# Kernel tuning notes

Measured on AMD Instinct MI355X. Metric: run time of the kernel, lower is better.

## Reference

```python
import jax, jax.numpy as jnp
import numpy as np

EMBED_DIM = 256
NUM_HEADS = 8
PROJ_DIM = EMBED_DIM // NUM_HEADS


def setup_inputs() -> dict:
    key = jax.random.key(0)
    ks = jax.random.split(key, 5)
    scale = 1.0 / np.sqrt(EMBED_DIM)
    inputs = jax.random.normal(ks[0], (2, 12, 12, 12, EMBED_DIM), dtype=jnp.float32)
    Wq = jax.random.normal(ks[1], (EMBED_DIM, EMBED_DIM), dtype=jnp.float32) * scale
    Wk = jax.random.normal(ks[2], (EMBED_DIM, EMBED_DIM), dtype=jnp.float32) * scale
    Wv = jax.random.normal(ks[3], (EMBED_DIM, EMBED_DIM), dtype=jnp.float32) * scale
    Wo = jax.random.normal(ks[4], (EMBED_DIM, EMBED_DIM), dtype=jnp.float32) * scale
    z = jnp.zeros((EMBED_DIM,), dtype=jnp.float32)
    return {"inputs": inputs, "Wq": Wq, "bq": z, "Wk": Wk, "bk": z,
            "Wv": Wv, "bv": z, "Wo": Wo, "bo": z}


def reference(inputs, Wq, bq, Wk, bk, Wv, bv, Wo, bo):
    B, h, w, d, E = inputs.shape
    S = h * w * d  # flattened spatial sequence
    x = inputs.reshape(B, S, E)
    # projections + head split: [B, S, E] -> [B, H, S, P]
    def split_heads(t):
        return t.reshape(B, S, NUM_HEADS, PROJ_DIM).transpose(0, 2, 1, 3)
    q = split_heads(x @ Wq + bq)
    k = split_heads(x @ Wk + bk)
    v = split_heads(x @ Wv + bv)
    # NOTE: original module does NOT scale by 1/sqrt(proj_dim)
    scores = jnp.einsum('bhsp,bhtp->bhst', q, k)  # [B, H, S, S]
    attn = jax.nn.softmax(scores, axis=-1)
    out = jnp.einsum('bhst,bhtp->bhsp', attn, v)  # [B, H, S, P]
    out = out.transpose(0, 2, 1, 3).reshape(B, h, w, d, E)
    return out @ Wo + bo
```

## Files before the change

kernel.cpp:

```cpp
#include <hip/hip_runtime.h>
#include <math.h>

#define EMBED 256
#define HEADS 8
#define PDIM  32
#define BATCH 2
#define SEQ   1728
#define NTOK  (BATCH*SEQ)
#define NE    (NTOK*EMBED)
#define KVB   128
#define NMAIN 13
#define TAIL0 1664
#define LOG2E 1.44269504088896f

typedef __attribute__((ext_vector_type(8))) __bf16 bf16x8;
typedef __attribute__((ext_vector_type(4))) float  f32x4;
typedef unsigned short ushort_t;
typedef unsigned int   uint_t;

static __device__ __forceinline__ unsigned short f2bf_rne(float f) {
    union { float f; unsigned u; } x; x.f = f;
    unsigned r = x.u + 0x7fffu + ((x.u >> 16) & 1u);
    return (unsigned short)(r >> 16);
}
union v8cast { uint4 u; bf16x8 v; };

static __device__ __forceinline__ void cvt8_hilo(const float f[8], bf16x8& hi, bf16x8& lo) {
    uint4 ph, pl;
    uint_t* phv = (uint_t*)&ph; uint_t* plv = (uint_t*)&pl;
    #pragma unroll
    for (int j = 0; j < 4; ++j) {
        const float f0 = f[2 * j], f1 = f[2 * j + 1];
        const uint_t u0 = __float_as_uint(f0) + 0x8000u;
        const uint_t u1 = __float_as_uint(f1) + 0x8000u;
        phv[j] = __builtin_amdgcn_perm(u1, u0, 0x07060302u);
        const float l0 = f0 - __uint_as_float(u0 & 0xFFFF0000u);
        const float l1 = f1 - __uint_as_float(u1 & 0xFFFF0000u);
        plv[j] = __builtin_amdgcn_perm(__float_as_uint(l1) + 0x8000u,
                                       __float_as_uint(l0) + 0x8000u, 0x07060302u);
    }
    v8cast ch; ch.u = ph; hi = ch.v;
    v8cast cl; cl.u = pl; lo = cl.v;
}

__global__ __launch_bounds__(256) void qkv_gemm_kernel(
    const float* __restrict__ x,
    const float* __restrict__ Wq, const float* __restrict__ bq,
    const float* __restrict__ Wk, const float* __restrict__ bk,
    const float* __restrict__ Wv, const float* __restrict__ bv,
    ushort_t* __restrict__ qo, ushort_t* __restrict__ ko, ushort_t* __restrict__ vt)
{
    const int t = threadIdx.x;
    const int lane = t & 63, li = lane & 15, quad = lane >> 4;
    const int w = t >> 6, wm = w >> 1, wn = w & 1;
    const int m0 = blockIdx.x * 64, n0 = blockIdx.y * 64, z = blockIdx.z;
    const float* __restrict__ W    = (z == 0) ? Wq : (z == 1) ? Wk : Wv;
    const float* __restrict__ bias = (z == 0) ? bq : (z == 1) ? bk : bv;

    __shared__ ushort_t Ah[2][64][40];
    __shared__ ushort_t Al[2][64][40];
    __shared__ ushort_t Bh[2][64][40];
    __shared__ ushort_t Bl[2][64][40];

    const int ar = t >> 2, ac = (t & 3) * 8;
    const int bn = t & 63, bk8 = (t >> 6) * 8;

    const float* agp = x + (size_t)(m0 + ar) * EMBED + ac;
    const float* bgp = W + (size_t)bk8 * EMBED + n0 + bn;

    float areg[8], breg[8];
    *(float4*)&areg[0] = *(const float4*)(agp);
    *(float4*)&areg[4] = *(const float4*)(agp + 4);
    #pragma unroll
    for (int j = 0; j < 8; ++j) breg[j] = bgp[(size_t)j * EMBED];

    f32x4 acc[2][2];
    #pragma unroll
    for (int mt = 0; mt < 2; ++mt)
        #pragma unroll
        for (int nt = 0; nt < 2; ++nt)
            acc[mt][nt] = (f32x4){0.f, 0.f, 0.f, 0.f};

    for (int ks = 0; ks < 8; ++ks) {
        const int p = ks & 1;
        {
            bf16x8 h, l;
            cvt8_hilo(areg, h, l);
            v8cast ch; ch.v = h; *(uint4*)&Ah[p][ar][ac] = ch.u;
            v8cast cl; cl.v = l; *(uint4*)&Al[p][ar][ac] = cl.u;
        }
        {
            bf16x8 h, l;
            cvt8_hilo(breg, h, l);
            v8cast ch; ch.v = h; *(uint4*)&Bh[p][bn][bk8] = ch.u;
            v8cast cl; cl.v = l; *(uint4*)&Bl[p][bn][bk8] = cl.u;
        }
        __syncthreads();
        if (ks < 7) {
            const int k1 = (ks + 1) * 32;
            *(float4*)&areg[0] = *(const float4*)(agp + k1);
            *(float4*)&areg[4] = *(const float4*)(agp + k1 + 4);
            const float* bg = bgp + (size_t)k1 * EMBED;
            #pragma unroll
            for (int j = 0; j < 8; ++j) breg[j] = bg[(size_t)j * EMBED];
        }
        bf16x8 ah[2], al_[2], bh[2], bl_[2];
        #pragma unroll
        for (int mt = 0; mt < 2; ++mt) {
            ah[mt]  = *(const bf16x8*)&Ah[p][wm * 32 + mt * 16 + li][quad * 8];
            al_[mt] = *(const bf16x8*)&Al[p][wm * 32 + mt * 16 + li][quad * 8];
        }
        #pragma unroll
        for (int nt = 0; nt < 2; ++nt) {
            bh[nt]  = *(const bf16x8*)&Bh[p][wn * 32 + nt * 16 + li][quad * 8];
            bl_[nt] = *(const bf16x8*)&Bl[p][wn * 32 + nt * 16 + li][quad * 8];
        }
        #pragma unroll
        for (int mt = 0; mt < 2; ++mt)
            #pragma unroll
            for (int nt = 0; nt < 2; ++nt) {
                acc[mt][nt] = __builtin_amdgcn_mfma_f32_16x16x32_bf16(ah[mt],  bh[nt],  acc[mt][nt], 0, 0, 0);
                acc[mt][nt] = __builtin_amdgcn_mfma_f32_16x16x32_bf16(al_[mt], bh[nt],  acc[mt][nt], 0, 0, 0);
                acc[mt][nt] = __builtin_amdgcn_mfma_f32_16x16x32_bf16(ah[mt],  bl_[nt], acc[mt][nt], 0, 0, 0);
            }
    }

    const int b = m0 / SEQ;
    const int sbase = m0 - b * SEQ + wm * 32;

    if (z <= 1) {
        ushort_t* __restrict__ dst = z ? ko : qo;
        #pragma unroll
        for (int nt = 0; nt < 2; ++nt) {
            const int gcol = n0 + wn * 32 + nt * 16 + li;
            const int h = gcol >> 5, p = gcol & 31;
            const float bb = bias[gcol];
            ushort_t* base = dst + ((size_t)(b * HEADS + h) * SEQ) * PDIM + p;
            #pragma unroll
            for (int mt = 0; mt < 2; ++mt)
                #pragma unroll
                for (int r = 0; r < 4; ++r) {
                    const int s = sbase + mt * 16 + quad * 4 + r;
                    base[(size_t)s * PDIM] = f2bf_rne(acc[mt][nt][r] + bb);
                }
        }
    } else {
        #pragma unroll
        for (int nt = 0; nt < 2; ++nt) {
            const int gcol = n0 + wn * 32 + nt * 16 + li;
            const int h = gcol >> 5, p = gcol & 31;
            const float bb = bias[gcol];
            ushort_t* base = vt + ((size_t)(b * HEADS + h) * PDIM + p) * SEQ;
            #pragma unroll
            for (int mt = 0; mt < 2; ++mt) {
                const int s0 = sbase + mt * 16 + quad * 4;
                ushort4 wv4;
                wv4.x = f2bf_rne(acc[mt][nt][0] + bb);
                wv4.y = f2bf_rne(acc[mt][nt][1] + bb);
                wv4.z = f2bf_rne(acc[mt][nt][2] + bb);
                wv4.w = f2bf_rne(acc[mt][nt][3] + bb);
                *(ushort4*)&base[s0] = wv4;
            }
        }
    }
}

__global__ __launch_bounds__(256) void attn_kernel(
    const ushort_t* __restrict__ q, const ushort_t* __restrict__ k,
    const ushort_t* __restrict__ vt, ushort_t* __restrict__ aob)
{
    const int t    = threadIdx.x;
    const int lane = t & 63;
    const int w    = t >> 6;
    const int li   = lane & 15;
    const int quad = lane >> 4;
    const int bid = blockIdx.x;
    const int g = bid & 7, j = bid >> 3;
    const int bh = g * 2 + (j >= 27 ? 1 : 0);
    const int qt = (j >= 27) ? (j - 27) : j;
    const int b  = bh >> 3, h = bh & 7;
    const int q0 = qt * 64 + w * 16;

    const ushort_t* __restrict__ qb = q  + (size_t)bh * SEQ * PDIM;
    const ushort_t* __restrict__ kb = k  + (size_t)bh * SEQ * PDIM;
    const ushort_t* __restrict__ vb = vt + (size_t)bh * PDIM * SEQ;

    __shared__ ushort_t Ks[2][128][40];
    __shared__ ushort_t Vs[2][32][136];
    __shared__ ushort_t Ps[4][16][136];

    const bf16x8 qfrag = *(const bf16x8*)(qb + (size_t)(q0 + li) * PDIM + quad * 8);

    const int krow = t >> 1, kcol = (t & 1) * 16;
    const int vrow = t >> 3, vkey = (t & 7) * 16;
    const ushort_t* kgp = kb + (size_t)krow * PDIM + kcol;
    const ushort_t* vgp = vb + (size_t)vrow * SEQ + vkey;

    f32x4 o0 = {0.f, 0.f, 0.f, 0.f};
    f32x4 o1 = {0.f, 0.f, 0.f, 0.f};
    float m_run = -__builtin_inff(), l_run = 0.f;

    uint4 ka  = *(const uint4*)(kgp);
    uint4 kc  = *(const uint4*)(kgp + 8);
    uint4 va  = *(const uint4*)(vgp);
    uint4 vc  = *(const uint4*)(vgp + 8);

    for (int it = 0; it < NMAIN; ++it) {
        const int p = it & 1;
        *(uint4*)&Ks[p][krow][kcol]     = ka;
        *(uint4*)&Ks[p][krow][kcol + 8] = kc;
        *(uint4*)&Vs[p][vrow][vkey]     = va;
        *(uint4*)&Vs[p][vrow][vkey + 8] = vc;
        __syncthreads();
        if (it + 1 < NMAIN) {
            const size_t ko = (size_t)(it + 1) * KVB * PDIM;
            ka = *(const uint4*)(kgp + ko);
            kc = *(const uint4*)(kgp + ko + 8);
            va = *(const uint4*)(vgp + (it + 1) * KVB);
            vc = *(const uint4*)(vgp + (it + 1) * KVB + 8);
        } else {
            const ushort_t* kt_ = kb + (size_t)(TAIL0 + (krow & 63)) * PDIM + kcol;
            ka = *(const uint4*)(kt_);
            kc = *(const uint4*)(kt_ + 8);
            const ushort_t* vt_ = vb + (size_t)vrow * SEQ + TAIL0 + (vkey & 63);
            va = *(const uint4*)(vt_);
            vc = *(const uint4*)(vt_ + 8);
        }

        const f32x4 zero = {0.f, 0.f, 0.f, 0.f};
        f32x4 st[8];
        #pragma unroll
        for (int jt = 0; jt < 8; ++jt) {
            const bf16x8 kf = *(const bf16x8*)&Ks[p][jt * 16 + li][quad * 8];
            st[jt] = __builtin_amdgcn_mfma_f32_16x16x32_bf16(kf, qfrag, zero, 0, 0, 0);
        }

        float tm = st[0][0];
        #pragma unroll
        for (int jt = 0; jt < 8; ++jt)
            #pragma unroll
            for (int r = 0; r < 4; ++r) tm = fmaxf(tm, st[jt][r]);
        tm = fmaxf(tm, __shfl_xor(tm, 16));
        tm = fmaxf(tm, __shfl_xor(tm, 32));
        const float mnew  = fmaxf(m_run, tm);
        const float negml = -(mnew * LOG2E);

        float ps = 0.f;
        #pragma unroll
        for (int jt = 0; jt < 8; ++jt) {
            const float p0 = __builtin_amdgcn_exp2f(fmaf(st[jt][0], LOG2E, negml));
            const float p1 = __builtin_amdgcn_exp2f(fmaf(st[jt][1], LOG2E, negml));
            const float p2 = __builtin_amdgcn_exp2f(fmaf(st[jt][2], LOG2E, negml));
            const float p3 = __builtin_amdgcn_exp2f(fmaf(st[jt][3], LOG2E, negml));
            ps += (p0 + p1) + (p2 + p3);
            uint2 pw;
            pw.x = __builtin_amdgcn_perm(__float_as_uint(p1) + 0x8000u,
                                         __float_as_uint(p0) + 0x8000u, 0x07060302u);
            pw.y = __builtin_amdgcn_perm(__float_as_uint(p3) + 0x8000u,
                                         __float_as_uint(p2) + 0x8000u, 0x07060302u);
            *(uint2*)&Ps[w][li][16 * jt + 4 * quad] = pw;
        }
        ps += __shfl_xor(ps, 16);
        ps += __shfl_xor(ps, 32);

        const float alpha = __builtin_amdgcn_exp2f(fmaf(m_run, LOG2E, negml));
        l_run = fmaf(l_run, alpha, ps);
        m_run = mnew;

        float af[4];
        #pragma unroll
        for (int r = 0; r < 4; ++r) af[r] = __shfl(alpha, 4 * quad + r);
        #pragma unroll
        for (int r = 0; r < 4; ++r) { o0[r] *= af[r]; o1[r] *= af[r]; }

        #pragma unroll
        for (int c = 0; c < 4; ++c) {
            const bf16x8 pa  = *(const bf16x8*)&Ps[w][li][32 * c + 8 * quad];
            const bf16x8 vf0 = *(const bf16x8*)&Vs[p][li][32 * c + quad * 8];
            const bf16x8 vf1 = *(const bf16x8*)&Vs[p][16 + li][32 * c + quad * 8];
            o0 = __builtin_amdgcn_mfma_f32_16x16x32_bf16(pa, vf0, o0, 0, 0, 0);
            o1 = __builtin_amdgcn_mfma_f32_16x16x32_bf16(pa, vf1, o1, 0, 0, 0);
        }
    }

    {
        const int p = NMAIN & 1;
        *(uint4*)&Ks[p][krow][kcol]     = ka;
        *(uint4*)&Ks[p][krow][kcol + 8] = kc;
        *(uint4*)&Vs[p][vrow][vkey]     = va;
        *(uint4*)&Vs[p][vrow][vkey + 8] = vc;
        __syncthreads();

        const f32x4 zero = {0.f, 0.f, 0.f, 0.f};
        f32x4 st[4];
        #pragma unroll
        for (int jt = 0; jt < 4; ++jt) {
            const bf16x8 kf = *(const bf16x8*)&Ks[p][jt * 16 + li][quad * 8];
            st[jt] = __builtin_amdgcn_mfma_f32_16x16x32_bf16(kf, qfrag, zero, 0, 0, 0);
        }

        float tm = st[0][0];
        #pragma unroll
        for (int jt = 0; jt < 4; ++jt)
            #pragma unroll
            for (int r = 0; r < 4; ++r) tm = fmaxf(tm, st[jt][r]);
        tm = fmaxf(tm, __shfl_xor(tm, 16));
        tm = fmaxf(tm, __shfl_xor(tm, 32));
        const float mnew  = fmaxf(m_run, tm);
        const float negml = -(mnew * LOG2E);

        float ps = 0.f;
        #pragma unroll
        for (int jt = 0; jt < 4; ++jt) {
            const float p0 = __builtin_amdgcn_exp2f(fmaf(st[jt][0], LOG2E, negml));
            const float p1 = __builtin_amdgcn_exp2f(fmaf(st[jt][1], LOG2E, negml));
            const float p2 = __builtin_amdgcn_exp2f(fmaf(st[jt][2], LOG2E, negml));
            const float p3 = __builtin_amdgcn_exp2f(fmaf(st[jt][3], LOG2E, negml));
            ps += (p0 + p1) + (p2 + p3);
            uint2 pw;
            pw.x = __builtin_amdgcn_perm(__float_as_uint(p1) + 0x8000u,
                                         __float_as_uint(p0) + 0x8000u, 0x07060302u);
            pw.y = __builtin_amdgcn_perm(__float_as_uint(p3) + 0x8000u,
                                         __float_as_uint(p2) + 0x8000u, 0x07060302u);
            *(uint2*)&Ps[w][li][16 * jt + 4 * quad] = pw;
        }
        ps += __shfl_xor(ps, 16);
        ps += __shfl_xor(ps, 32);

        const float alpha = __builtin_amdgcn_exp2f(fmaf(m_run, LOG2E, negml));
        l_run = fmaf(l_run, alpha, ps);
        m_run = mnew;

        float af[4];
        #pragma unroll
        for (int r = 0; r < 4; ++r) af[r] = __shfl(alpha, 4 * quad + r);
        #pragma unroll
        for (int r = 0; r < 4; ++r) { o0[r] *= af[r]; o1[r] *= af[r]; }

        #pragma unroll
        for (int c = 0; c < 2; ++c) {
            const bf16x8 pa  = *(const bf16x8*)&Ps[w][li][32 * c + 8 * quad];
            const bf16x8 vf0 = *(const bf16x8*)&Vs[p][li][32 * c + quad * 8];
            const bf16x8 vf1 = *(const bf16x8*)&Vs[p][16 + li][32 * c + quad * 8];
            o0 = __builtin_amdgcn_mfma_f32_16x16x32_bf16(pa, vf0, o0, 0, 0, 0);
            o1 = __builtin_amdgcn_mfma_f32_16x16x32_bf16(pa, vf1, o1, 0, 0, 0);
        }
    }

    float linv[4];
    #pragma unroll
    for (int r = 0; r < 4; ++r) linv[r] = 1.0f / __shfl(l_run, 4 * quad + r);
    #pragma unroll
    for (int r = 0; r < 4; ++r) {
        const int s = q0 + 4 * quad + r;
        ushort_t* row = aob + ((size_t)(b * SEQ + s)) * EMBED + h * PDIM;
        row[li]      = f2bf_rne(o0[r] * linv[r]);
        row[16 + li] = f2bf_rne(o1[r] * linv[r]);
    }
}

__global__ __launch_bounds__(64) void out_gemm_kernel(
    const ushort_t* __restrict__ a, const float* __restrict__ Wo,
    const float* __restrict__ bo, float* __restrict__ out)
{
    const int lane = threadIdx.x, li = lane & 15, quad = lane >> 4;
    const int m0 = blockIdx.x * 32, n0 = blockIdx.y * 16;

    const ushort_t* aph = a + (size_t)(m0 + li) * EMBED + quad * 8;

    f32x4 acc[2];
    #pragma unroll
    for (int mt = 0; mt < 2; ++mt) acc[mt] = (f32x4){0.f, 0.f, 0.f, 0.f};

    #pragma unroll 2
    for (int k0 = 0; k0 < EMBED; k0 += 32) {
        bf16x8 ah[2];
        #pragma unroll
        for (int mt = 0; mt < 2; ++mt)
            ah[mt] = *(const bf16x8*)(aph + (size_t)mt * 16 * EMBED + k0);
        const float* wp = Wo + (size_t)(k0 + quad * 8) * EMBED + n0 + li;
        uint4 pb;
        uint_t* pbv = (uint_t*)&pb;
        #pragma unroll
        for (int j = 0; j < 4; ++j) {
            const uint_t u0 = __float_as_uint(wp[(size_t)(2 * j) * EMBED])     + 0x8000u;
            const uint_t u1 = __float_as_uint(wp[(size_t)(2 * j + 1) * EMBED]) + 0x8000u;
            pbv[j] = __builtin_amdgcn_perm(u1, u0, 0x07060302u);
        }
        v8cast cb; cb.u = pb;
        #pragma unroll
        for (int mt = 0; mt < 2; ++mt)
            acc[mt] = __builtin_amdgcn_mfma_f32_16x16x32_bf16(ah[mt], cb.v, acc[mt], 0, 0, 0);
    }

    const float bb = bo[n0 + li];
    #pragma unroll
    for (int mt = 0; mt < 2; ++mt)
        #pragma unroll
        for (int r = 0; r < 4; ++r) {
            const int row = m0 + mt * 16 + quad * 4 + r;
            out[(size_t)row * EMBED + n0 + li] = acc[mt][r] + bb;
        }
}

extern "C" void kernel_launch(void* const* d_in, const int* in_sizes, int n_in,
                              void* d_out, int out_size, void* d_ws, size_t ws_size,
                              hipStream_t stream)
{
    const float* x  = (const float*)d_in[0];
    const float* Wq = (const float*)d_in[1];
    const float* bq = (const float*)d_in[2];
    const float* Wk = (const float*)d_in[3];
    const float* bk = (const float*)d_in[4];
    const float* Wv = (const float*)d_in[5];
    const float* bv = (const float*)d_in[6];
    const float* Wo = (const float*)d_in[7];
    const float* bo = (const float*)d_in[8];
    float* out = (float*)d_out;

    ushort_t* ws  = (ushort_t*)d_ws;
    ushort_t* qb  = ws;
    ushort_t* kb  = qb + (size_t)NE;
    ushort_t* vt  = kb + (size_t)NE;
    ushort_t* aob = vt + (size_t)NE;

    qkv_gemm_kernel<<<dim3(NTOK / 64, EMBED / 64, 3), 256, 0, stream>>>(
        x, Wq, bq, Wk, bk, Wv, bv, qb, kb, vt);
    attn_kernel<<<dim3(432), 256, 0, stream>>>(qb, kb, vt, aob);
    out_gemm_kernel<<<dim3(NTOK / 32, 16), 64, 0, stream>>>(aob, Wo, bo, out);
}
```

Before: 113.7 us.

## Split attention KV range across paired waves and stage Wo tile in LDS

The attention kernel doubles the block to 512 threads so two waves share each 16-query group, each processing half of the key/value sequence in 64-key tiles. Their partial softmax states are merged through shared memory at the end. This targets the long serial KV loop and low wave count per CU, at the cost of an extra reduction step, more LDS and idle iterations for one half. Separately, the output GEMM now uses 256-thread blocks that convert a Wo column tile to bf16 once into LDS instead of every wave re-reading and converting fp32 weights each k-step.

After: 113.6 us. About the same (-0.0%).

```diff
diff --git a/kernel.cpp b/kernel.cpp
--- a/kernel.cpp
+++ b/kernel.cpp
@@ -8,9 +8,6 @@
 #define SEQ   1728
 #define NTOK  (BATCH*SEQ)
 #define NE    (NTOK*EMBED)
-#define KVB   128
-#define NMAIN 13
-#define TAIL0 1664
 #define LOG2E 1.44269504088896f
 
 typedef __attribute__((ext_vector_type(8))) __bf16 bf16x8;
@@ -165,7 +162,7 @@
     }
 }
 
-__global__ __launch_bounds__(256) void attn_kernel(
+__global__ __launch_bounds__(512, 4) void attn_kernel(
     const ushort_t* __restrict__ q, const ushort_t* __restrict__ k,
     const ushort_t* __restrict__ vt, ushort_t* __restrict__ aob)
 {
@@ -174,197 +171,171 @@
     const int w    = t >> 6;
     const int li   = lane & 15;
     const int quad = lane >> 4;
+    const int qg   = w >> 1, half = w & 1;
     const int bid = blockIdx.x;
     const int g = bid & 7, j = bid >> 3;
     const int bh = g * 2 + (j >= 27 ? 1 : 0);
     const int qt = (j >= 27) ? (j - 27) : j;
     const int b  = bh >> 3, h = bh & 7;
-    const int q0 = qt * 64 + w * 16;
+    const int q0 = qt * 64 + qg * 16;
 
     const ushort_t* __restrict__ qb = q  + (size_t)bh * SEQ * PDIM;
     const ushort_t* __restrict__ kb = k  + (size_t)bh * SEQ * PDIM;
     const ushort_t* __restrict__ vb = vt + (size_t)bh * PDIM * SEQ;
 
-    __shared__ ushort_t Ks[2][128][40];
-    __shared__ ushort_t Vs[2][32][136];
-    __shared__ ushort_t Ps[4][16][136];
+    __shared__ __align__(16) char SMRAW[57344];
+    ushort_t (*Ks)[2][64][40] = reinterpret_cast<ushort_t (*)[2][64][40]>(SMRAW);
+    ushort_t (*Vs)[2][32][72] = reinterpret_cast<ushort_t (*)[2][32][72]>(SMRAW + 20480);
+    ushort_t (*Ps)[16][72]    = reinterpret_cast<ushort_t (*)[16][72]>(SMRAW + 38912);
+    float    (*Om)[16][33]    = reinterpret_cast<float (*)[16][33]>(SMRAW + 38912);
+    float    (*Ml)[2][16]     = reinterpret_cast<float (*)[2][16]>(SMRAW);
 
     const bf16x8 qfrag = *(const bf16x8*)(qb + (size_t)(q0 + li) * PDIM + quad * 8);
 
-    const int krow = t >> 1, kcol = (t & 1) * 16;
-    const int vrow = t >> 3, vkey = (t & 7) * 16;
-    const ushort_t* kgp = kb + (size_t)krow * PDIM + kcol;
-    const ushort_t* vgp = vb + (size_t)vrow * SEQ + vkey;
+    const int ts = t & 255, hstage = t >> 8;
+    const int krow = ts >> 2, kc = (ts & 3) * 8;
+    const int vrow = ts >> 3, vk = (ts & 7) * 8;
+    const int tb = hstage ? 896 : 0;
 
     f32x4 o0 = {0.f, 0.f, 0.f, 0.f};
     f32x4 o1 = {0.f, 0.f, 0.f, 0.f};
     float m_run = -__builtin_inff(), l_run = 0.f;
 
-    uint4 ka  = *(const uint4*)(kgp);
-    uint4 kc  = *(const uint4*)(kgp + 8);
-    uint4 va  = *(const uint4*)(vgp);
-    uint4 vc  = *(const uint4*)(vgp + 8);
-
-    for (int it = 0; it < NMAIN; ++it) {
+    uint4 kreg = *(const uint4*)(kb + (size_t)(tb + krow) * PDIM + kc);
+    uint4 vreg = *(const uint4*)(vb + (size_t)vrow * SEQ + tb + vk);
+
+    const int myn = half ? 13 : 14;
+
+    for (int it = 0; it < 14; ++it) {
         const int p = it & 1;
-        *(uint4*)&Ks[p][krow][kcol]     = ka;
-        *(uint4*)&Ks[p][krow][kcol + 8] = kc;
-        *(uint4*)&Vs[p][vrow][vkey]     = va;
-        *(uint4*)&Vs[p][vrow][vkey + 8] = vc;
+        *(uint4*)&Ks[p][hstage][krow][kc] = kreg;
+        *(uint4*)&Vs[p][hstage][vrow][vk] = vreg;
         __syncthreads();
-        if (it + 1 < NMAIN) {
-            const size_t ko = (size_t)(it + 1) * KVB * PDIM;
-            ka = *(const uint4*)(kgp + ko);
-            kc = *(const uint4*)(kgp + ko + 8);
-            va = *(const uint4*)(vgp + (it + 1) * KVB);
-            vc = *(const uint4*)(vgp + (it + 1) * KVB + 8);
-        } else {
-            const ushort_t* kt_ = kb + (size_t)(TAIL0 + (krow & 63)) * PDIM + kcol;
-            ka = *(const uint4*)(kt_);
-            kc = *(const uint4*)(kt_ + 8);
-            const ushort_t* vt_ = vb + (size_t)vrow * SEQ + TAIL0 + (vkey & 63);
-            va = *(const uint4*)(vt_);
-            vc = *(const uint4*)(vt_ + 8);
-        }
-
-        const f32x4 zero = {0.f, 0.f, 0.f, 0.f};
-        f32x4 st[8];
-        #pragma unroll
-        for (int jt = 0; jt < 8; ++jt) {
-            const bf16x8 kf = *(const bf16x8*)&Ks[p][jt * 16 + li][quad * 8];
-            st[jt] = __builtin_amdgcn_mfma_f32_16x16x32_bf16(kf, qfrag, zero, 0, 0, 0);
-        }
-
-        float tm = st[0][0];
-        #pragma unroll
-        for (int jt = 0; jt < 8; ++jt)
-            #pragma unroll
-            for (int r = 0; r < 4; ++r) tm = fmaxf(tm, st[jt][r]);
-        tm = fmaxf(tm, __shfl_xor(tm, 16));
-        tm = fmaxf(tm, __shfl_xor(tm, 32));
-        const float mnew  = fmaxf(m_run, tm);
-        const float negml = -(mnew * LOG2E);
-
-        float ps = 0.f;
-        #pragma unroll
-        for (int jt = 0; jt < 8; ++jt) {
-            const float p0 = __builtin_amdgcn_exp2f(fmaf(st[jt][0], LOG2E, negml));
-            const float p1 = __builtin_amdgcn_exp2f(fmaf(st[jt][1], LOG2E, negml));
-            const float p2 = __builtin_amdgcn_exp2f(fmaf(st[jt][2], LOG2E, negml));
-            const float p3 = __builtin_amdgcn_exp2f(fmaf(st[jt][3], LOG2E, negml));
-            ps += (p0 + p1) + (p2 + p3);
-            uint2 pw;
-            pw.x = __builtin_amdgcn_perm(__float_as_uint(p1) + 0x8000u,
-                                         __float_as_uint(p0) + 0x8000u, 0x07060302u);
-            pw.y = __builtin_amdgcn_perm(__float_as_uint(p3) + 0x8000u,
-                                         __float_as_uint(p2) + 0x8000u, 0x07060302u);
-            *(uint2*)&Ps[w][li][16 * jt + 4 * quad] = pw;
-        }
-        ps += __shfl_xor(ps, 16);
-        ps += __shfl_xor(ps, 32);
-
-        const float alpha = __builtin_amdgcn_exp2f(fmaf(m_run, LOG2E, negml));
-        l_run = fmaf(l_run, alpha, ps);
-        m_run = mnew;
-
-        float af[4];
-        #pragma unroll
-        for (int r = 0; r < 4; ++r) af[r] = __shfl(alpha, 4 * quad + r);
-        #pragma unroll
-        for (int r = 0; r < 4; ++r) { o0[r] *= af[r]; o1[r] *= af[r]; }
-
-        #pragma unroll
-        for (int c = 0; c < 4; ++c) {
-            const bf16x8 pa  = *(const bf16x8*)&Ps[w][li][32 * c + 8 * quad];
-            const bf16x8 vf0 = *(const bf16x8*)&Vs[p][li][32 * c + quad * 8];
-            const bf16x8 vf1 = *(const bf16x8*)&Vs[p][16 + li][32 * c + quad * 8];
-            o0 = __builtin_amdgcn_mfma_f32_16x16x32_bf16(pa, vf0, o0, 0, 0, 0);
-            o1 = __builtin_amdgcn_mfma_f32_16x16x32_bf16(pa, vf1, o1, 0, 0, 0);
-        }
-    }
-
-    {
-        const int p = NMAIN & 1;
-        *(uint4*)&Ks[p][krow][kcol]     = ka;
-        *(uint4*)&Ks[p][krow][kcol + 8] = kc;
-        *(uint4*)&Vs[p][vrow][vkey]     = va;
-        *(uint4*)&Vs[p][vrow][vkey + 8] = vc;
-        __syncthreads();
-
-        const f32x4 zero = {0.f, 0.f, 0.f, 0.f};
-        f32x4 st[4];
-        #pragma unroll
-        for (int jt = 0; jt < 4; ++jt) {
-            const bf16x8 kf = *(const bf16x8*)&Ks[p][jt * 16 + li][quad * 8];
-            st[jt] = __builtin_amdgcn_mfma_f32_16x16x32_bf16(kf, qfrag, zero, 0, 0, 0);
-        }
-
-        float tm = st[0][0];
-        #pragma unroll
-        for (int jt = 0; jt < 4; ++jt)
-            #pragma unroll
-            for (int r = 0; r < 4; ++r) tm = fmaxf(tm, st[jt][r]);
-        tm = fmaxf(tm, __shfl_xor(tm, 16));
-        tm = fmaxf(tm, __shfl_xor(tm, 32));
-        const float mnew  = fmaxf(m_run, tm);
-        const float negml = -(mnew * LOG2E);
-
-        float ps = 0.f;
-        #pragma unroll
-        for (int jt = 0; jt < 4; ++jt) {
-            const float p0 = __builtin_amdgcn_exp2f(fmaf(st[jt][0], LOG2E, negml));
-            const float p1 = __builtin_amdgcn_exp2f(fmaf(st[jt][1], LOG2E, negml));
-            const float p2 = __builtin_amdgcn_exp2f(fmaf(st[jt][2], LOG2E, negml));
-            const float p3 = __builtin_amdgcn_exp2f(fmaf(st[jt][3], LOG2E, negml));
-            ps += (p0 + p1) + (p2 + p3);
-            uint2 pw;
-            pw.x = __builtin_amdgcn_perm(__float_as_uint(p1) + 0x8000u,
-                                         __float_as_uint(p0) + 0x8000u, 0x07060302u);
-            pw.y = __builtin_amdgcn_perm(__float_as_uint(p3) + 0x8000u,
-                                         __float_as_uint(p2) + 0x8000u, 0x07060302u);
-            *(uint2*)&Ps[w][li][16 * jt + 4 * quad] = pw;
-        }
-        ps += __shfl_xor(ps, 16);
-        ps += __shfl_xor(ps, 32);
-
-        const float alpha = __builtin_amdgcn_exp2f(fmaf(m_run, LOG2E, negml));
-        l_run = fmaf(l_run, alpha, ps);
-        m_run = mnew;
-
-        float af[4];
-        #pragma unroll
-        for (int r = 0; r < 4; ++r) af[r] = __shfl(alpha, 4 * quad + r);
-        #pragma unroll
-        for (int r = 0; r < 4; ++r) { o0[r] *= af[r]; o1[r] *= af[r]; }
-
-        #pragma unroll
-        for (int c = 0; c < 2; ++c) {
-            const bf16x8 pa  = *(const bf16x8*)&Ps[w][li][32 * c + 8 * quad];
-            const bf16x8 vf0 = *(const bf16x8*)&Vs[p][li][32 * c + quad * 8];
-            const bf16x8 vf1 = *(const bf16x8*)&Vs[p][16 + li][32 * c + quad * 8];
-            o0 = __builtin_amdgcn_mfma_f32_16x16x32_bf16(pa, vf0, o0, 0, 0, 0);
-            o1 = __builtin_amdgcn_mfma_f32_16x16x32_bf16(pa, vf1, o1, 0, 0, 0);
-        }
-    }
-
-    float linv[4];
-    #pragma unroll
-    for (int r = 0; r < 4; ++r) linv[r] = 1.0f / __shfl(l_run, 4 * quad + r);
+        if (it + 1 < 14) {
+            const int nt_ = it + 1;
+            const int t1 = hstage ? (14 + nt_ > 26 ? 26 : 14 + nt_) : nt_;
+            kreg = *(const uint4*)(kb + (size_t)(t1 * 64 + krow) * PDIM + kc);
+            vreg = *(const uint4*)(vb + (size_t)vrow * SEQ + t1 * 64 + vk);
+        }
+
+        if (it < myn) {
+            const f32x4 zero = {0.f, 0.f, 0.f, 0.f};
+            f32x4 st[4];
+            #pragma unroll
+            for (int jt = 0; jt < 4; ++jt) {
+                const bf16x8 kf = *(const bf16x8*)&Ks[p][half][jt * 16 + li][quad * 8];
+                st[jt] = __builtin_amdgcn_mfma_f32_16x16x32_bf16(kf, qfrag, zero, 0, 0, 0);
+            }
+
+            float tm = st[0][0];
+            #pragma unroll
+            for (int jt = 0; jt < 4; ++jt)
+                #pragma unroll
+                for (int r = 0; r < 4; ++r) tm = fmaxf(tm, st[jt][r]);
+            tm = fmaxf(tm, __shfl_xor(tm, 16));
+            tm = fmaxf(tm, __shfl_xor(tm, 32));
+            const float mnew  = fmaxf(m_run, tm);
+            const float negml = -(mnew * LOG2E);
+
+            float ps = 0.f;
+            #pragma unroll
+            for (int jt = 0; jt < 4; ++jt) {
+                const float p0 = __builtin_amdgcn_exp2f(fmaf(st[jt][0], LOG2E, negml));
+                const float p1 = __builtin_amdgcn_exp2f(fmaf(st[jt][1], LOG2E, negml));
+                const float p2 = __builtin_amdgcn_exp2f(fmaf(st[jt][2], LOG2E, negml));
+                const float p3 = __builtin_amdgcn_exp2f(fmaf(st[jt][3], LOG2E, negml));
+                ps += (p0 + p1) + (p2 + p3);
+                uint2 pw;
+                pw.x = __builtin_amdgcn_perm(__float_as_uint(p1) + 0x8000u,
+                                             __float_as_uint(p0) + 0x8000u, 0x07060302u);
+                pw.y = __builtin_amdgcn_perm(__float_as_uint(p3) + 0x8000u,
+                                             __float_as_uint(p2) + 0x8000u, 0x07060302u);
+                *(uint2*)&Ps[w][li][16 * jt + 4 * quad] = pw;
+            }
+            ps += __shfl_xor(ps, 16);
+            ps += __shfl_xor(ps, 32);
+
+            const float alpha = __builtin_amdgcn_exp2f(fmaf(m_run, LOG2E, negml));
+            l_run = fmaf(l_run, alpha, ps);
+            m_run = mnew;
+
+            float af[4];
+            #pragma unroll
+            for (int r = 0; r < 4; ++r) af[r] = __shfl(alpha, 4 * quad + r);
+            #pragma unroll
+            for (int r = 0; r < 4; ++r) { o0[r] *= af[r]; o1[r] *= af[r]; }
+
+            const bf16x8 pa0 = *(const bf16x8*)&Ps[w][li][8 * quad];
+            const bf16x8 pa1 = *(const bf16x8*)&Ps[w][li][32 + 8 * quad];
+            const bf16x8 vf00 = *(const bf16x8*)&Vs[p][half][li][quad * 8];
+            const bf16x8 vf01 = *(const bf16x8*)&Vs[p][half][16 + li][quad * 8];
+            const bf16x8 vf10 = *(const bf16x8*)&Vs[p][half][li][32 + quad * 8];
+            const bf16x8 vf11 = *(const bf16x8*)&Vs[p][half][16 + li][32 + quad * 8];
+            o0 = __builtin_amdgcn_mfma_f32_16x16x32_bf16(pa0, vf00, o0, 0, 0, 0);
+            o0 = __builtin_amdgcn_mfma_f32_16x16x32_bf16(pa1, vf10, o0, 0, 0, 0);
+            o1 = __builtin_amdgcn_mfma_f32_16x16x32_bf16(pa0, vf01, o1, 0, 0, 0);
+            o1 = __builtin_amdgcn_mfma_f32_16x16x32_bf16(pa1, vf11, o1, 0, 0, 0);
+        }
+    }
+
+    __syncthreads();
     #pragma unroll
     for (int r = 0; r < 4; ++r) {
-        const int s = q0 + 4 * quad + r;
-        ushort_t* row = aob + ((size_t)(b * SEQ + s)) * EMBED + h * PDIM;
-        row[li]      = f2bf_rne(o0[r] * linv[r]);
-        row[16 + li] = f2bf_rne(o1[r] * linv[r]);
-    }
-}
-
-__global__ __launch_bounds__(64) void out_gemm_kernel(
+        Om[w][4 * quad + r][li]      = o0[r];
+        Om[w][4 * quad + r][16 + li] = o1[r];
+    }
+    if (quad == 0) { Ml[w][0][li] = m_run; Ml[w][1][li] = l_run; }
+    __syncthreads();
+
+    const int wa = qg * 2, wb = wa + 1;
+    const float ma = Ml[wa][0][li], mb = Ml[wb][0][li];
+    const float mC = fmaxf(ma, mb);
+    const float sa = __builtin_amdgcn_exp2f((ma - mC) * LOG2E);
+    const float sb = __builtin_amdgcn_exp2f((mb - mC) * LOG2E);
+    const float lC = Ml[wa][1][li] * sa + Ml[wb][1][li] * sb;
+    const float inv = 1.0f / lC;
+    const float fa = sa * inv, fb = sb * inv;
+    const int c = half * 16 + li;
+    #pragma unroll
+    for (int r = 0; r < 4; ++r) {
+        const int qq = 4 * quad + r;
+        const float aq  = __shfl(fa, qq);
+        const float bq_ = __shfl(fb, qq);
+        const float val = Om[wa][qq][c] * aq + Om[wb][qq][c] * bq_;
+        const int s = q0 + qq;
+        aob[((size_t)(b * SEQ + s)) * EMBED + h * PDIM + c] = f2bf_rne(val);
+    }
+}
+
+__global__ __launch_bounds__(256) void out_gemm_kernel(
     const ushort_t* __restrict__ a, const float* __restrict__ Wo,
     const float* __restrict__ bo, float* __restrict__ out)
 {
-    const int lane = threadIdx.x, li = lane & 15, quad = lane >> 4;
-    const int m0 = blockIdx.x * 32, n0 = blockIdx.y * 16;
+    const int t = threadIdx.x;
+    const int lane = t & 63, li = lane & 15, quad = lane >> 4;
+    const int w = t >> 6;
+    const int m0 = blockIdx.x * 128 + w * 32, n0 = blockIdx.y * 16;
+
+    __shared__ ushort_t Bh[16][260];
+
+    {
+        const int n = t & 15, kc = (t >> 4) * 16;
+        const float* wp = Wo + (size_t)kc * EMBED + n0 + n;
+        uint4 q0v, q1v;
+        uint_t* b0 = (uint_t*)&q0v; uint_t* b1 = (uint_t*)&q1v;
+        #pragma unroll
+        for (int j = 0; j < 4; ++j) {
+            const uint_t u0 = __float_as_uint(wp[(size_t)(2 * j) * EMBED])     + 0x8000u;
+            const uint_t u1 = __float_as_uint(wp[(size_t)(2 * j + 1) * EMBED]) + 0x8000u;
+            b0[j] = __builtin_amdgcn_perm(u1, u0, 0x07060302u);
+            const uint_t u2 = __float_as_uint(wp[(size_t)(8 + 2 * j) * EMBED])     + 0x8000u;
+            const uint_t u3 = __float_as_uint(wp[(size_t)(8 + 2 * j + 1) * EMBED]) + 0x8000u;
+            b1[j] = __builtin_amdgcn_perm(u3, u2, 0x07060302u);
+        }
+        *(uint4*)&Bh[n][kc]     = q0v;
+        *(uint4*)&Bh[n][kc + 8] = q1v;
+    }
+    __syncthreads();
 
     const ushort_t* aph = a + (size_t)(m0 + li) * EMBED + quad * 8;
 
@@ -378,19 +349,10 @@
         #pragma unroll
         for (int mt = 0; mt < 2; ++mt)
             ah[mt] = *(const bf16x8*)(aph + (size_t)mt * 16 * EMBED + k0);
-        const float* wp = Wo + (size_t)(k0 + quad * 8) * EMBED + n0 + li;
-        uint4 pb;
-        uint_t* pbv = (uint_t*)&pb;
-        #pragma unroll
-        for (int j = 0; j < 4; ++j) {
-            const uint_t u0 = __float_as_uint(wp[(size_t)(2 * j) * EMBED])     + 0x8000u;
-            const uint_t u1 = __float_as_uint(wp[(size_t)(2 * j + 1) * EMBED]) + 0x8000u;
-            pbv[j] = __builtin_amdgcn_perm(u1, u0, 0x07060302u);
-        }
-        v8cast cb; cb.u = pb;
+        const bf16x8 bf = *(const bf16x8*)&Bh[li][k0 + quad * 8];
         #pragma unroll
         for (int mt = 0; mt < 2; ++mt)
-            acc[mt] = __builtin_amdgcn_mfma_f32_16x16x32_bf16(ah[mt], cb.v, acc[mt], 0, 0, 0);
+            acc[mt] = __builtin_amdgcn_mfma_f32_16x16x32_bf16(ah[mt], bf, acc[mt], 0, 0, 0);
     }
 
     const float bb = bo[n0 + li];
@@ -426,6 +388,6 @@
 
     qkv_gemm_kernel<<<dim3(NTOK / 64, EMBED / 64, 3), 256, 0, stream>>>(
         x, Wq, bq, Wk, bk, Wv, bv, qb, kb, vt);
-    attn_kernel<<<dim3(432), 256, 0, stream>>>(qb, kb, vt, aob);
-    out_gemm_kernel<<<dim3(NTOK / 32, 16), 64, 0, stream>>>(aob, Wo, bo, out);
-}
+    attn_kernel<<<dim3(432), 512, 0, stream>>>(qb, kb, vt, aob);
+    out_gemm_kernel<<<dim3(NTOK / 128, 16), 256, 0, stream>>>(aob, Wo, bo, out);
+}
```
